# Performance work log

Hardware: AMD Instinct MI355X
Metric: run time of the kernel (lower is better)

Reference implementation:

```python
import jax, jax.numpy as jnp
import numpy as np

CONF_THR = 0.5   # hard-coded `confidence` in pre_process_pred
NMS_THR = 0.5    # hard-coded `nms_conf` in pre_process_pred
IMG = 608.0


def setup_inputs() -> dict:
    key = jax.random.key(0)
    k1, k2, k3 = jax.random.split(key, 3)
    B, N, C = 16, 2048, 80
    u = jax.random.uniform(k1, (B, N, 4), dtype=jnp.float32)
    # cx, cy in [0, 608); w, h in [2, 120) pixels (YOLO-style pixel coords, matches +1 IoU convention)
    pred_boxes = jnp.concatenate([u[..., :2] * IMG, 2.0 + u[..., 2:] * 118.0], axis=-1)
    pred_objectness = jax.random.uniform(k2, (B, N, 1), dtype=jnp.float32)
    pred_logits = jax.random.uniform(k3, (B, N, C), dtype=jnp.float32)
    return {"pred_boxes": pred_boxes, "pred_objectness": pred_objectness, "pred_logits": pred_logits}


def _pairwise_iou(b):
    # b: [N,4] xyxy; +1 pixel convention exactly as original bbox_iou
    x1 = jnp.maximum(b[:, None, 0], b[None, :, 0])
    y1 = jnp.maximum(b[:, None, 1], b[None, :, 1])
    x2 = jnp.minimum(b[:, None, 2], b[None, :, 2])
    y2 = jnp.minimum(b[:, None, 3], b[None, :, 3])
    inter = jnp.clip(x2 - x1 + 1.0, 0.0) * jnp.clip(y2 - y1 + 1.0, 0.0)
    area = (b[:, 2] - b[:, 0] + 1.0) * (b[:, 3] - b[:, 1] + 1.0)
    return inter / (area[:, None] + area[None, :] - inter)


def _nms_one(boxes, obj, logits):
    # boxes: [N,4] cxcywh, obj: [N], logits: [N,C]
    N = boxes.shape[0]
    cx, cy, w, h = boxes[:, 0], boxes[:, 1], boxes[:, 2], boxes[:, 3]
    xyxy = jnp.stack([cx - w / 2, cy - h / 2, cx + w / 2, cy + h / 2], axis=-1)
    valid = obj > CONF_THR                    # confidence gate (strict >, as in original)
    cls_conf = jnp.max(logits, axis=-1)       # max_conf
    cls = jnp.argmax(logits, axis=-1)         # max_conf_score (class index)
    # sort by objectness descending; invalid boxes pushed to the end
    score = jnp.where(valid, obj, -jnp.inf)
    order = jnp.argsort(-score)
    xyxy_s = xyxy[order]
    obj_s = obj[order]
    valid_s = valid[order]
    cls_s = cls[order]
    conf_s = cls_conf[order]
    iou = _pairwise_iou(jax.lax.stop_gradient(xyxy_s))   # [N,N]
    same = cls_s[:, None] == cls_s[None, :]              # per-class NMS grouping
    idx = jnp.arange(N)

    def body(i, alive):
        # a box suppresses only if it is itself still alive & valid (greedy removal semantics)
        sup = alive[i] & valid_s[i] & (iou[i] >= NMS_THR) & same[i] & (idx > i)
        return alive & ~sup

    alive = jax.lax.fori_loop(0, N, body, valid_s)
    keep = alive & valid_s
    det = jnp.concatenate(
        [xyxy_s, obj_s[:, None], conf_s[:, None], cls_s.astype(xyxy_s.dtype)[:, None]], axis=-1
    )  # [N,7] = (x1,y1,x2,y2,obj,cls_conf,cls)
    return jnp.where(keep[:, None], det, 0.0)


def reference(pred_boxes, pred_objectness, pred_logits):
    obj = pred_objectness[..., 0]
    dets = jax.vmap(_nms_one)(pred_boxes, obj, pred_logits)  # [B,N,7]
    B, N, _ = dets.shape
    bind = jnp.broadcast_to(jnp.arange(B, dtype=dets.dtype)[:, None, None], (B, N, 1))
    # [B,N,8]: (batch_ind, x1,y1,x2,y2, obj, cls_conf, cls); suppressed rows are all-zero padding
    return jnp.concatenate([bind, dets], axis=-1)
```

## Files before the change

### kernel.cpp

```cpp
#include <hip/hip_runtime.h>
#include <stdint.h>

#define BB 16
#define NN 2048
#define CC 80
#define CONF_THRV 0.5f
#define NMS_THRV 0.5f

__global__ __launch_bounds__(256) void k_rank_all(
    const float4* __restrict__ boxes,
    const float* __restrict__ obj,
    const float* __restrict__ logits,
    float4* __restrict__ sxyxy,
    float* __restrict__ sarea,
    float* __restrict__ sobj,
    float* __restrict__ sconf,
    int* __restrict__ scls,
    int* __restrict__ nvalid) {
  __shared__ unsigned long long lk[NN];
  __shared__ int cnt;
  int b = blockIdx.y;
  int t = threadIdx.x;
  if (t == 0) cnt = 0;
  __syncthreads();
  size_t base = (size_t)b * NN;
  int myv = 0;
  #pragma unroll
  for (int r = 0; r < NN / 256; ++r) {
    int a = t + r * 256;
    float o = obj[base + a];
    bool v = o > CONF_THRV;
    float s = v ? o : -INFINITY;
    unsigned u = __float_as_uint(s);
    u = (u & 0x80000000u) ? ~u : (u | 0x80000000u);
    lk[a] = ((unsigned long long)u << 32) |
            (unsigned long long)(0xFFFFFFFFu - (unsigned)a);
    myv += v ? 1 : 0;
  }
  atomicAdd(&cnt, myv);
  __syncthreads();
  if (t == 0) nvalid[b] = cnt;

  int i = blockIdx.x * 256 + t;
  unsigned long long ki = lk[i];
  const unsigned long long VK = (0xBF000000ull << 32) | 0xFFFFFFFFull;
  if (ki <= VK) return;

  int rank = 0;
  const ulonglong2* lk2 = (const ulonglong2*)lk;
  #pragma unroll 4
  for (int j = 0; j < NN / 2; j += 2) {
    ulonglong2 a2 = lk2[j];
    ulonglong2 c2 = lk2[j + 1];
    rank += (a2.x > ki) + (a2.y > ki) + (c2.x > ki) + (c2.y > ki);
  }

  const float4* lp = (const float4*)(logits + (base + i) * CC);
  float best = -INFINITY;
  int bi = 0;
  #pragma unroll
  for (int q = 0; q < CC / 4; ++q) {
    float4 v4 = lp[q];
    if (v4.x > best) { best = v4.x; bi = 4 * q + 0; }
    if (v4.y > best) { best = v4.y; bi = 4 * q + 1; }
    if (v4.z > best) { best = v4.z; bi = 4 * q + 2; }
    if (v4.w > best) { best = v4.w; bi = 4 * q + 3; }
  }

  float4 bx = boxes[base + i];
  float hw = bx.z / 2.0f, hh = bx.w / 2.0f;
  float x1 = bx.x - hw, y1 = bx.y - hh;
  float x2 = bx.x + hw, y2 = bx.y + hh;
  sxyxy[base + rank] = make_float4(x1, y1, x2, y2);
  sarea[base + rank] = __fmul_rn(x2 - x1 + 1.0f, y2 - y1 + 1.0f);
  sobj[base + rank] = obj[base + i];
  sconf[base + rank] = best;
  scls[base + rank] = bi;
}

__global__ void k_masks(const float4* __restrict__ sxyxy,
                        const float* __restrict__ sarea,
                        const int* __restrict__ scls,
                        const int* __restrict__ nvalid,
                        uint32_t* __restrict__ masksT) {
  int b = blockIdx.y;
  int pair = blockIdx.x * blockDim.x + threadIdx.x;
  int i = pair & (NN - 1);
  int w = pair >> 11;
  int nv = nvalid[b];
  int nwords = (nv + 31) >> 5;
  if (w >= nwords) return;
  size_t base = (size_t)b * NN;
  uint32_t bits = 0;
  int j0 = w * 32;
  int jend = min(j0 + 32, nv);
  int jstart = max(j0, i + 1);
  if (i < nv && jstart < jend) {
    float4 bi = sxyxy[base + i];
    float ai = sarea[base + i];
    int ci = scls[base + i];
    for (int j = jstart; j < jend; ++j) {
      float4 bj = sxyxy[base + j];
      float xx1 = fmaxf(bi.x, bj.x);
      float yy1 = fmaxf(bi.y, bj.y);
      float xx2 = fminf(bi.z, bj.z);
      float yy2 = fminf(bi.w, bj.w);
      float cw = fmaxf(xx2 - xx1 + 1.0f, 0.0f);
      float ch = fmaxf(yy2 - yy1 + 1.0f, 0.0f);
      float inter = __fmul_rn(cw, ch);
      float aj = sarea[base + j];
      float denom = (ai + aj) - inter;
      float iou = inter / denom;
      if (iou >= NMS_THRV && scls[base + j] == ci) bits |= (1u << (j - j0));
    }
  }
  masksT[((size_t)b * 64 + w) * NN + i] = bits;
}

__global__ __launch_bounds__(512) void k_scan_write(
    const uint32_t* __restrict__ masksT,
    const int* __restrict__ nvalid,
    const float4* __restrict__ sxyxy,
    const float* __restrict__ sobj,
    const float* __restrict__ sconf,
    const int* __restrict__ scls,
    float* __restrict__ out) {
  __shared__ uint32_t rsh[64];
  int b = blockIdx.x;
  int t = threadIdx.x;
  int nv = nvalid[b];

  if (t < 64) {
    int lane = t;
    int nwords = (nv + 31) >> 5;
    int nch4 = (nwords + 3) & ~3;
    bool act = lane < nwords;
    const uint4* col = (const uint4*)(masksT + ((size_t)b * 64 + lane) * NN);
    uint32_t remv = 0;
    uint4 z4; z4.x = z4.y = z4.z = z4.w = 0u;
    uint4 A[8], B[8], C[8], D[8];
    #pragma unroll
    for (int q = 0; q < 8; ++q) { A[q] = z4; B[q] = z4; C[q] = z4; D[q] = z4; }
#define LOADBUF(BUF, CH) do {                                          \
      if (act) {                                                       \
        int rr = (CH) < 64 ? (CH) : 0;                                 \
        _Pragma("unroll")                                              \
        for (int q = 0; q < 8; ++q) BUF[q] = col[rr * 8 + q];          \
      }                                                                \
    } while (0)
    LOADBUF(A, 0); LOADBUF(B, 1); LOADBUF(C, 2); LOADBUF(D, 3);
#define STEP(BUF, CH, RCH) do {                                        \
      uint32_t cur[32];                                                \
      _Pragma("unroll")                                                \
      for (int q = 0; q < 8; ++q) {                                    \
        cur[4*q+0] = BUF[q].x; cur[4*q+1] = BUF[q].y;                  \
        cur[4*q+2] = BUF[q].z; cur[4*q+3] = BUF[q].w;                  \
      }                                                                \
      LOADBUF(BUF, RCH);                                               \
      uint32_t all_or = 0;                                             \
      _Pragma("unroll")                                                \
      for (int d = 0; d < 32; ++d) all_or |= cur[d];                   \
      uint32_t word_c = (uint32_t)__shfl((int)remv, (CH), 64);         \
      uint32_t diag   = (uint32_t)__shfl((int)all_or, (CH), 64);       \
      if (diag == 0u) {                                                \
        if (word_c == 0u) {                                            \
          remv |= all_or;                                              \
        } else {                                                       \
          uint32_t acc = 0;                                            \
          _Pragma("unroll")                                            \
          for (int d = 0; d < 32; ++d)                                 \
            acc |= ((word_c >> d) & 1u) ? 0u : cur[d];                 \
          remv |= acc;                                                 \
        }                                                              \
      } else {                                                         \
        uint32_t wc = word_c, acc = 0;                                 \
        _Pragma("unroll")                                              \
        for (int d = 0; d < 32; ++d) {                                 \
          uint32_t dd = (uint32_t)__shfl((int)cur[d], (CH), 64);       \
          if (((wc >> d) & 1u) == 0u) { wc |= dd; acc |= cur[d]; }     \
        }                                                              \
        remv |= acc;                                                   \
      }                                                                \
    } while (0)
    for (int c = 0; c < nch4; c += 4) {
      STEP(A, c + 0, c + 4);
      STEP(B, c + 1, c + 5);
      STEP(C, c + 2, c + 6);
      STEP(D, c + 3, c + 7);
    }
#undef STEP
#undef LOADBUF
    rsh[lane] = remv;
  }
  __syncthreads();

  #pragma unroll
  for (int rep = 0; rep < 4; ++rep) {
    int r = t + rep * 512;
    size_t idx = (size_t)b * NN + r;
    bool keep = false;
    if (r < nv) {
      uint32_t wrd = rsh[r >> 5];
      keep = !((wrd >> (r & 31)) & 1u);
    }
    float4 xy = make_float4(0.f, 0.f, 0.f, 0.f);
    float o = 0.f, cf = 0.f, cl = 0.f;
    if (keep) {
      xy = sxyxy[idx];
      o = sobj[idx];
      cf = sconf[idx];
      cl = (float)scls[idx];
    }
    float4* op = (float4*)(out + idx * 8);
    op[0] = make_float4((float)b, xy.x, xy.y, xy.z);
    op[1] = make_float4(xy.w, o, cf, cl);
  }
}

extern "C" void kernel_launch(void* const* d_in, const int* in_sizes, int n_in,
                              void* d_out, int out_size, void* d_ws, size_t ws_size,
                              hipStream_t stream) {
  const float4* boxes = (const float4*)d_in[0];
  const float* obj = (const float*)d_in[1];
  const float* logits = (const float*)d_in[2];
  float* out = (float*)d_out;

  char* ws = (char*)d_ws;
  size_t off = 0;
  float4* sxyxy = (float4*)(ws + off);            off += (size_t)BB * NN * 16;
  float* sarea = (float*)(ws + off);              off += (size_t)BB * NN * 4;
  float* sobj = (float*)(ws + off);               off += (size_t)BB * NN * 4;
  float* sconf = (float*)(ws + off);              off += (size_t)BB * NN * 4;
  int* scls = (int*)(ws + off);                   off += (size_t)BB * NN * 4;
  int* nvalid = (int*)(ws + off);                 off += 256;
  uint32_t* masksT = (uint32_t*)(ws + off);       off += (size_t)BB * NN * 64 * 4;

  hipLaunchKernelGGL(k_rank_all, dim3(NN / 256, BB), dim3(256), 0, stream,
                     boxes, obj, logits,
                     sxyxy, sarea, sobj, sconf, scls, nvalid);
  hipLaunchKernelGGL(k_masks, dim3(NN * 64 / 256, BB), dim3(256), 0, stream,
                     sxyxy, sarea, scls, nvalid, masksT);
  hipLaunchKernelGGL(k_scan_write, dim3(BB), dim3(512), 0, stream,
                     masksT, nvalid, sxyxy, sobj, sconf, scls, out);
}
```

Before: 148.2 us.

## Compact valid boxes via wave ballot before rank counting in k_rank_all

The ranking kernel now uses one 64-thread wavefront per block that stream-compacts only the confidence-passing boxes into shared memory with ballot/popcount, then ranks each valid key against only the compacted count instead of all 2048 keys. The original index and objectness are decoded from the key, which removes a global reload of obj. Each block still redundantly loads the whole obj row and builds the compacted list serially across 32 iterations. The grid is 32 blocks of 64 threads per batch instead of 8 blocks of 256.

```diff
diff --git a/kernel.cpp b/kernel.cpp
--- a/kernel.cpp
+++ b/kernel.cpp
@@ -7,7 +7,7 @@
 #define CONF_THRV 0.5f
 #define NMS_THRV 0.5f
 
-__global__ __launch_bounds__(256) void k_rank_all(
+__global__ __launch_bounds__(64) void k_rank_all(
     const float4* __restrict__ boxes,
     const float* __restrict__ obj,
     const float* __restrict__ logits,
@@ -17,43 +17,48 @@
     float* __restrict__ sconf,
     int* __restrict__ scls,
     int* __restrict__ nvalid) {
-  __shared__ unsigned long long lk[NN];
-  __shared__ int cnt;
+  __shared__ unsigned long long lk[NN + 4];
   int b = blockIdx.y;
   int t = threadIdx.x;
-  if (t == 0) cnt = 0;
-  __syncthreads();
   size_t base = (size_t)b * NN;
-  int myv = 0;
-  #pragma unroll
-  for (int r = 0; r < NN / 256; ++r) {
-    int a = t + r * 256;
+  unsigned long long mlt = (1ull << t) - 1ull;
+
+  int run = 0;
+  #pragma unroll 8
+  for (int r = 0; r < NN / 64; ++r) {
+    int a = r * 64 + t;
     float o = obj[base + a];
     bool v = o > CONF_THRV;
-    float s = v ? o : -INFINITY;
-    unsigned u = __float_as_uint(s);
-    u = (u & 0x80000000u) ? ~u : (u | 0x80000000u);
-    lk[a] = ((unsigned long long)u << 32) |
-            (unsigned long long)(0xFFFFFFFFu - (unsigned)a);
-    myv += v ? 1 : 0;
-  }
-  atomicAdd(&cnt, myv);
+    unsigned long long m = __ballot(v);
+    if (v) {
+      unsigned u = __float_as_uint(o) | 0x80000000u;
+      lk[run + __popcll(m & mlt)] =
+          ((unsigned long long)u << 32) |
+          (unsigned long long)(0xFFFFFFFFu - (unsigned)a);
+    }
+    run += __popcll(m);
+  }
+  int nv = run;
+  if (t < 4) lk[nv + t] = 0ull;
+  if (blockIdx.x == 0 && t == 0) nvalid[b] = nv;
   __syncthreads();
-  if (t == 0) nvalid[b] = cnt;
-
-  int i = blockIdx.x * 256 + t;
-  unsigned long long ki = lk[i];
-  const unsigned long long VK = (0xBF000000ull << 32) | 0xFFFFFFFFull;
-  if (ki <= VK) return;
+
+  int s = blockIdx.x * 64 + t;
+  if (s >= nv) return;
+  unsigned long long ki = lk[s];
 
   int rank = 0;
+  int nvr = (nv + 3) & ~3;
   const ulonglong2* lk2 = (const ulonglong2*)lk;
   #pragma unroll 4
-  for (int j = 0; j < NN / 2; j += 2) {
+  for (int j = 0; j < nvr / 2; j += 2) {
     ulonglong2 a2 = lk2[j];
     ulonglong2 c2 = lk2[j + 1];
     rank += (a2.x > ki) + (a2.y > ki) + (c2.x > ki) + (c2.y > ki);
   }
+
+  int i = (int)(0xFFFFFFFFu - (unsigned)(ki & 0xFFFFFFFFull));
+  float oi = __uint_as_float((unsigned)(ki >> 32) & 0x7FFFFFFFu);
 
   const float4* lp = (const float4*)(logits + (base + i) * CC);
   float best = -INFINITY;
@@ -73,7 +78,7 @@
   float x2 = bx.x + hw, y2 = bx.y + hh;
   sxyxy[base + rank] = make_float4(x1, y1, x2, y2);
   sarea[base + rank] = __fmul_rn(x2 - x1 + 1.0f, y2 - y1 + 1.0f);
-  sobj[base + rank] = obj[base + i];
+  sobj[base + rank] = oi;
   sconf[base + rank] = best;
   scls[base + rank] = bi;
 }
@@ -235,7 +240,7 @@
   int* nvalid = (int*)(ws + off);                 off += 256;
   uint32_t* masksT = (uint32_t*)(ws + off);       off += (size_t)BB * NN * 64 * 4;
 
-  hipLaunchKernelGGL(k_rank_all, dim3(NN / 256, BB), dim3(256), 0, stream,
+  hipLaunchKernelGGL(k_rank_all, dim3(32, BB), dim3(64), 0, stream,
                      boxes, obj, logits,
                      sxyxy, sarea, sobj, sconf, scls, nvalid);
   hipLaunchKernelGGL(k_masks, dim3(NN * 64 / 256, BB), dim3(256), 0, stream,
```

After: 145.8 us. No clear change (-1.6%).
